# Kernel optimization log

Hardware: AMD Instinct MI355X
Metric: run time of the kernel (lower is better)

The kernel has to match this reference:

```python
import jax, jax.numpy as jnp
import numpy as np

N, F, E, LIN, C, B = 16384, 500, 128, 128, 10, 4096
P_EDGE = 0.002  # ~32 avg degree


def _l2norm(x):
    # F.normalize(dim=1), eps=1e-12
    n = jnp.linalg.norm(x, axis=1, keepdims=True)
    return x / jnp.maximum(n, 1e-12)


def setup_inputs() -> dict:
    key = jax.random.key(0)
    ks = jax.random.split(key, 10)
    adj = (jax.random.uniform(ks[0], (N, N)) < P_EDGE).astype(jnp.float32)
    idx = jnp.arange(N)
    adj = adj.at[idx, idx].set(1.0)  # self-loops guarantee degree >= 1
    data = jax.random.normal(ks[1], (N, F), dtype=jnp.float32)
    nodes = jax.random.randint(ks[2], (B,), 0, N)
    # Encoder 1: Linear(2F -> E); Encoder 2: Linear(2E -> E); classifier heads
    W1 = jax.random.normal(ks[3], (E, 2 * F), dtype=jnp.float32) * 0.03
    b1 = jnp.zeros((E,), jnp.float32)
    W2 = jax.random.normal(ks[4], (E, 2 * E), dtype=jnp.float32) * 0.06
    b2 = jnp.zeros((E,), jnp.float32)
    Wl1 = jax.random.normal(ks[5], (LIN, E), dtype=jnp.float32) * 0.08
    bl1 = jnp.zeros((LIN,), jnp.float32)
    Wl2 = jax.random.normal(ks[6], (C, LIN), dtype=jnp.float32) * 0.12
    bl2 = jnp.zeros((C,), jnp.float32)
    return {"nodes": nodes, "adj": adj, "data": data,
            "W1": W1, "b1": b1, "W2": W2, "b2": b2,
            "Wl1": Wl1, "bl1": bl1, "Wl2": Wl2, "bl2": bl2}


def reference(nodes, adj, data, W1, b1, W2, b2, Wl1, bl1, Wl2, bl2):
    deg = jnp.sum(adj, axis=1, keepdims=True)  # [N,1]
    # Layer 1 (mean aggregator over full neighbor set): computed for all nodes
    neigh1 = (adj @ data) / deg                               # [N,F]
    h1 = jnp.concatenate([data, neigh1], axis=1)              # [N,2F] (self, neigh)
    H1 = _l2norm(jax.nn.relu(h1 @ W1.T + b1))                 # [N,E]
    # Layer 2: only for the queried node batch
    neigh2 = (adj[nodes] @ H1) / deg[nodes]                   # [B,E]
    h2 = jnp.concatenate([H1[nodes], neigh2], axis=1)         # [B,2E]
    H2 = _l2norm(jax.nn.relu(h2 @ W2.T + b2))                 # [B,E]
    x = H2 @ Wl1.T + bl1                                      # [B,LIN]
    x = x @ Wl2.T + bl2                                       # [B,C]
    return jax.nn.softmax(x, axis=1)
```

## Files before the change

kernel.cpp:

```cpp
#include <hip/hip_runtime.h>
#include <math.h>
#include <stddef.h>

#define N_NODES 16384
#define F_DIM   500
#define KP1     512
#define E_DIM   128
#define C_DIM   10
#define B_DIM   4096
#define MAXDEG  128

typedef __attribute__((ext_vector_type(8))) short short8;
typedef __attribute__((ext_vector_type(4))) float f32x4;

__device__ inline unsigned short f2bf(float f) {
    union { float f; unsigned int u; } v; v.f = f;
    unsigned int u = v.u;
    u += 0x7FFFu + ((u >> 16) & 1u);
    return (unsigned short)(u >> 16);
}
__device__ inline float bf2f(unsigned short u) {
    union { unsigned int u; float f; } v; v.u = (unsigned int)u << 16;
    return v.f;
}

__global__ __launch_bounds__(256) void k_prep(const float* __restrict__ W1,
                                              const float* __restrict__ W2,
                                              const float* __restrict__ Wl1,
                                              unsigned short* __restrict__ Wt1,
                                              unsigned short* __restrict__ W2ab16,
                                              unsigned short* __restrict__ W2bb16,
                                              float* __restrict__ Wl1t) {
    const int bb = blockIdx.x;
    const int t = threadIdx.x;
    if (bb < 512) {
        int idx = bb * 256 + t;
        int n = idx >> 9, k = idx & 511;
        float v = (k < F_DIM) ? W1[(size_t)(n & 127) * 1000 + (n >> 7) * F_DIM + k] : 0.0f;
        Wt1[idx] = f2bf(v);
    } else if (bb < 576) {
        int idx = (bb - 512) * 256 + t;
        int n = idx >> 7, k = idx & 127;
        W2ab16[idx] = f2bf(W2[(size_t)n * 256 + k]);
    } else if (bb < 640) {
        int idx = (bb - 576) * 256 + t;
        int n = idx >> 7, k = idx & 127;
        W2bb16[idx] = f2bf(W2[(size_t)n * 256 + 128 + k]);
    } else {
        __shared__ float tile[32][33];
        int tb = bb - 640;
        int k0 = (tb & 3) * 32, e0 = (tb >> 2) * 32;
        int tx = t & 31, ty0 = t >> 5;
#pragma unroll
        for (int q = 0; q < 4; ++q) {
            int ty = ty0 + q * 8;
            tile[ty][tx] = Wl1[(size_t)(e0 + ty) * 128 + k0 + tx];
        }
        __syncthreads();
#pragma unroll
        for (int q = 0; q < 4; ++q) {
            int ty = ty0 + q * 8;
            Wl1t[(size_t)(k0 + ty) * 128 + e0 + tx] = tile[tx][ty];
        }
    }
}

__global__ __launch_bounds__(256) void k_mix(const float* __restrict__ data,
                                             const unsigned short* __restrict__ Wt1,
                                             unsigned short* __restrict__ Xb16,
                                             const float* __restrict__ adj,
                                             unsigned short* __restrict__ nbr,
                                             int* __restrict__ deg) {
    __shared__ alignas(16) unsigned char s_raw[(32 * 40 + 256 * 40) * 2];
    const int bb = blockIdx.x;
    const int tid = threadIdx.x;

    if (bb < 512) {
        unsigned short* sA = (unsigned short*)s_raw;
        unsigned short* sB = sA + 32 * 40;
        const int w    = tid >> 6;
        const int lane = tid & 63;
        const int l16  = lane & 15;
        const int quad = lane >> 4;
        const int blockM = bb * 32;
        f32x4 acc[2][4] = {};
#pragma unroll 1
        for (int c = 0; c < (KP1 >> 5); ++c) {
            const int k0 = c << 5;
            if (tid < 128) {
                int row = tid >> 2, cc = tid & 3;
                int kbase = k0 + cc * 8;
                const float* Arow = data + (size_t)(blockM + row) * F_DIM;
                float4 f0 = (kbase + 4 <= F_DIM) ? *(const float4*)(Arow + kbase)
                                                 : make_float4(0.f, 0.f, 0.f, 0.f);
                float4 f1 = (kbase + 8 <= F_DIM) ? *(const float4*)(Arow + kbase + 4)
                                                 : make_float4(0.f, 0.f, 0.f, 0.f);
                short8 v;
                v[0] = (short)f2bf(f0.x); v[1] = (short)f2bf(f0.y);
                v[2] = (short)f2bf(f0.z); v[3] = (short)f2bf(f0.w);
                v[4] = (short)f2bf(f1.x); v[5] = (short)f2bf(f1.y);
                v[6] = (short)f2bf(f1.z); v[7] = (short)f2bf(f1.w);
                *(short8*)(sA + row * 40 + cc * 8) = v;
            }
#pragma unroll
            for (int q = 0; q < 4; ++q) {
                int idx = tid + 256 * q;
                int row = idx >> 2, cc = idx & 3;
                short8 v = *(const short8*)(Wt1 + (size_t)row * KP1 + k0 + cc * 8);
                *(short8*)(sB + row * 40 + cc * 8) = v;
            }
            __syncthreads();
            short8 af[2], bf[4];
#pragma unroll
            for (int mt = 0; mt < 2; ++mt)
                af[mt] = *(const short8*)(sA + (mt * 16 + l16) * 40 + quad * 8);
#pragma unroll
            for (int nt = 0; nt < 4; ++nt)
                bf[nt] = *(const short8*)(sB + (w * 64 + nt * 16 + l16) * 40 + quad * 8);
#pragma unroll
            for (int mt = 0; mt < 2; ++mt)
#pragma unroll
                for (int nt = 0; nt < 4; ++nt)
                    acc[mt][nt] = __builtin_amdgcn_mfma_f32_16x16x32_bf16(af[mt], bf[nt], acc[mt][nt], 0, 0, 0);
            __syncthreads();
        }
#pragma unroll
        for (int mt = 0; mt < 2; ++mt)
#pragma unroll
            for (int nt = 0; nt < 4; ++nt) {
                int col = w * 64 + nt * 16 + l16;
#pragma unroll
                for (int r = 0; r < 4; ++r) {
                    int row = blockM + mt * 16 + quad * 4 + r;
                    Xb16[(size_t)row * 256 + col] = f2bf(acc[mt][nt][r]);
                }
            }
    } else {
        const int i = bb - 512;
        int* s_cnt = (int*)s_raw;
        int* s_idx = ((int*)s_raw) + 4;
        const float4* row4 = (const float4*)(adj + (size_t)i * N_NODES);
        if (tid == 0) *s_cnt = 0;
        __syncthreads();
        float4 v[16];
#pragma unroll
        for (int p = 0; p < 16; ++p) v[p] = row4[p * 256 + tid];
#pragma unroll
        for (int p = 0; p < 16; ++p) {
            int col = p * 1024 + tid * 4;
            if (v[p].x != 0.f) { int q = atomicAdd(s_cnt, 1); if (q < MAXDEG) s_idx[q] = col;     }
            if (v[p].y != 0.f) { int q = atomicAdd(s_cnt, 1); if (q < MAXDEG) s_idx[q] = col + 1; }
            if (v[p].z != 0.f) { int q = atomicAdd(s_cnt, 1); if (q < MAXDEG) s_idx[q] = col + 2; }
            if (v[p].w != 0.f) { int q = atomicAdd(s_cnt, 1); if (q < MAXDEG) s_idx[q] = col + 3; }
        }
        __syncthreads();
        int cnt = *s_cnt; if (cnt > MAXDEG) cnt = MAXDEG;
        if (tid < cnt) nbr[(size_t)i * MAXDEG + tid] = (unsigned short)s_idx[tid];
        if (tid == 0) deg[i] = cnt;
    }
}

__global__ __launch_bounds__(256) void k_gather(const unsigned short* __restrict__ nbr,
                                                const int* __restrict__ deg,
                                                const unsigned short* __restrict__ Xb16,
                                                const float* __restrict__ b1,
                                                unsigned short* __restrict__ H1b) {
    const int i = blockIdx.x;
    const int t = threadIdx.x;
    const int cnt = deg[i];
    __shared__ int s_idx[MAXDEG];
    __shared__ float s_part[8][128];
    __shared__ float s_w[2];
    if (t < cnt) s_idx[t] = nbr[(size_t)i * MAXDEG + t];
    __syncthreads();
    const int g = t >> 5, l = t & 31;
    float4 a4 = make_float4(0.f, 0.f, 0.f, 0.f);
    for (int k = g; k < cnt; k += 8) {
        ushort4 x4 = ((const ushort4*)(Xb16 + (size_t)s_idx[k] * 256 + 128))[l];
        a4.x += bf2f(x4.x); a4.y += bf2f(x4.y); a4.z += bf2f(x4.z); a4.w += bf2f(x4.w);
    }
    *(float4*)&s_part[g][l * 4] = a4;
    __syncthreads();
    float vv = 0.f;
    if (t < 128) {
        float tot = 0.f;
#pragma unroll
        for (int g2 = 0; g2 < 8; ++g2) tot += s_part[g2][t];
        vv = bf2f(Xb16[(size_t)i * 256 + t]) + tot / (float)cnt + b1[t];
        vv = fmaxf(vv, 0.f);
        float s = vv * vv;
#pragma unroll
        for (int off = 32; off > 0; off >>= 1) s += __shfl_down(s, off, 64);
        if ((t & 63) == 0) s_w[t >> 6] = s;
    }
    __syncthreads();
    if (t < 128) {
        float denom = fmaxf(sqrtf(s_w[0] + s_w[1]), 1e-12f);
        H1b[(size_t)i * 128 + t] = f2bf(vv / denom);
    }
}

__global__ __launch_bounds__(256) void k_gemm2(const unsigned short* __restrict__ H1b,
                                               const unsigned short* __restrict__ W2bb16,
                                               const unsigned short* __restrict__ W2ab16,
                                               const int* __restrict__ nodes,
                                               unsigned short* __restrict__ Yb16,
                                               float* __restrict__ Ya) {
    __shared__ unsigned short sA[32 * 40];
    __shared__ unsigned short sB[128 * 40];
    const int bb = blockIdx.x;
    const bool selfp = (bb >= 512);
    const unsigned short* B = selfp ? W2ab16 : W2bb16;
    const int blockM = (selfp ? (bb - 512) : bb) * 32;
    const int tid  = threadIdx.x;
    const int w    = tid >> 6;
    const int lane = tid & 63;
    const int l16  = lane & 15;
    const int quad = lane >> 4;
    f32x4 acc[2][2] = {};
#pragma unroll
    for (int c = 0; c < 4; ++c) {
        const int k0 = c << 5;
        if (tid < 128) {
            int row = tid >> 2, cc = tid & 3;
            int m = blockM + row;
            int src = selfp ? nodes[m] : m;
            short8 v = *(const short8*)(H1b + (size_t)src * 128 + k0 + cc * 8);
            *(short8*)(sA + row * 40 + cc * 8) = v;
        }
#pragma unroll
        for (int q = 0; q < 2; ++q) {
            int idx = tid + 256 * q;
            int row = idx >> 2, cc = idx & 3;
            short8 v = *(const short8*)(B + (size_t)row * 128 + k0 + cc * 8);
            *(short8*)(sB + row * 40 + cc * 8) = v;
        }
        __syncthreads();
        short8 af[2], bf[2];
#pragma unroll
        for (int mt = 0; mt < 2; ++mt)
            af[mt] = *(const short8*)(sA + (mt * 16 + l16) * 40 + quad * 8);
#pragma unroll
        for (int nt = 0; nt < 2; ++nt)
            bf[nt] = *(const short8*)(sB + (w * 32 + nt * 16 + l16) * 40 + quad * 8);
#pragma unroll
        for (int mt = 0; mt < 2; ++mt)
#pragma unroll
            for (int nt = 0; nt < 2; ++nt)
                acc[mt][nt] = __builtin_amdgcn_mfma_f32_16x16x32_bf16(af[mt], bf[nt], acc[mt][nt], 0, 0, 0);
        __syncthreads();
    }
#pragma unroll
    for (int mt = 0; mt < 2; ++mt)
#pragma unroll
        for (int nt = 0; nt < 2; ++nt) {
            int col = w * 32 + nt * 16 + l16;
#pragma unroll
            for (int r = 0; r < 4; ++r) {
                int row = blockM + mt * 16 + quad * 4 + r;
                if (selfp) Ya[(size_t)row * 128 + col] = acc[mt][nt][r];
                else       Yb16[(size_t)row * 128 + col] = f2bf(acc[mt][nt][r]);
            }
        }
}

__global__ __launch_bounds__(256) void k_l2head(const int* __restrict__ nodes,
                                                const unsigned short* __restrict__ nbr,
                                                const int* __restrict__ deg,
                                                const unsigned short* __restrict__ Yb16,
                                                const float* __restrict__ Ya,
                                                const float* __restrict__ b2,
                                                const float* __restrict__ Wl1t,
                                                const float* __restrict__ bl1,
                                                const float* __restrict__ Wl2,
                                                const float* __restrict__ bl2,
                                                float* __restrict__ out) {
    const int b = blockIdx.x;
    const int t = threadIdx.x;
    const int n = nodes[b];
    const int cnt = deg[n];
    __shared__ int s_idx[MAXDEG];
    __shared__ float s_part[8][128];
    __shared__ float s_h[128];
    __shared__ float s_x[128];
    __shared__ float s_c[C_DIM];
    __shared__ float s_w[2];
    if (t < cnt) s_idx[t] = nbr[(size_t)n * MAXDEG + t];
    __syncthreads();
    const int g = t >> 5, l = t & 31;
    float4 a4 = make_float4(0.f, 0.f, 0.f, 0.f);
    for (int k = g; k < cnt; k += 8) {
        ushort4 y4 = ((const ushort4*)(Yb16 + (size_t)s_idx[k] * 128))[l];
        a4.x += bf2f(y4.x); a4.y += bf2f(y4.y); a4.z += bf2f(y4.z); a4.w += bf2f(y4.w);
    }
    *(float4*)&s_part[g][l * 4] = a4;
    __syncthreads();
    float vv = 0.f;
    if (t < 128) {
        float tot = 0.f;
#pragma unroll
        for (int g2 = 0; g2 < 8; ++g2) tot += s_part[g2][t];
        vv = Ya[(size_t)b * 128 + t] + tot / (float)cnt + b2[t];
        vv = fmaxf(vv, 0.f);
        float s = vv * vv;
#pragma unroll
        for (int off = 32; off > 0; off >>= 1) s += __shfl_down(s, off, 64);
        if ((t & 63) == 0) s_w[t >> 6] = s;
    }
    __syncthreads();
    if (t < 128) {
        float denom = fmaxf(sqrtf(s_w[0] + s_w[1]), 1e-12f);
        s_h[t] = vv / denom;
    }
    __syncthreads();
    if (t < 128) {
        float x1 = bl1[t];
#pragma unroll 8
        for (int kk = 0; kk < 128; ++kk)
            x1 += Wl1t[kk * 128 + t] * s_h[kk];
        s_x[t] = x1;
    }
    __syncthreads();
    if (t < C_DIM) {
        float l2 = bl2[t];
        const float* wr = Wl2 + (size_t)t * 128;
        for (int kk = 0; kk < 128; ++kk) l2 += wr[kk] * s_x[kk];
        s_c[t] = l2;
    }
    __syncthreads();
    if (t < C_DIM) {
        float mx = -1e30f;
        for (int c = 0; c < C_DIM; ++c) mx = fmaxf(mx, s_c[c]);
        float se = 0.f;
        for (int c = 0; c < C_DIM; ++c) se += expf(s_c[c] - mx);
        out[(size_t)b * C_DIM + t] = expf(s_c[t] - mx) / se;
    }
}

extern "C" void kernel_launch(void* const* d_in, const int* in_sizes, int n_in,
                              void* d_out, int out_size, void* d_ws, size_t ws_size,
                              hipStream_t stream) {
    const int*   nodes = (const int*)  d_in[0];
    const float* adj   = (const float*)d_in[1];
    const float* data  = (const float*)d_in[2];
    const float* W1    = (const float*)d_in[3];
    const float* b1    = (const float*)d_in[4];
    const float* W2    = (const float*)d_in[5];
    const float* b2    = (const float*)d_in[6];
    const float* Wl1   = (const float*)d_in[7];
    const float* bl1   = (const float*)d_in[8];
    const float* Wl2   = (const float*)d_in[9];
    const float* bl2   = (const float*)d_in[10];
    float* out = (float*)d_out;

    float* Wl1t = (float*)d_ws;
    float* Ya   = Wl1t + 16384;
    unsigned short* Wt1    = (unsigned short*)(Ya + (size_t)B_DIM * 128);
    unsigned short* W2ab16 = Wt1 + 256 * KP1;
    unsigned short* W2bb16 = W2ab16 + 16384;
    unsigned short* Xb16   = W2bb16 + 16384;
    unsigned short* H1b    = Xb16 + (size_t)N_NODES * 256;
    unsigned short* Yb16   = H1b + (size_t)N_NODES * 128;
    unsigned short* nbr    = Yb16 + (size_t)N_NODES * 128;
    int* deg = (int*)(nbr + (size_t)N_NODES * MAXDEG);

    k_prep<<<656, 256, 0, stream>>>(W1, W2, Wl1, Wt1, W2ab16, W2bb16, Wl1t);

    k_mix   <<<512 + N_NODES, 256, 0, stream>>>(data, Wt1, Xb16, adj, nbr, deg);
    k_gather<<<N_NODES, 256, 0, stream>>>(nbr, deg, Xb16, b1, H1b);

    k_gemm2 <<<512 + 128, 256, 0, stream>>>(H1b, W2bb16, W2ab16, nodes, Yb16, Ya);

    k_l2head<<<B_DIM, 256, 0, stream>>>(nodes, nbr, deg, Yb16, Ya, b2,
                                        Wl1t, bl1, Wl2, bl2, out);
}
```

Before: 1.419 ms.

## Fuse weight prep into first GEMM and use wave-per-node gather and head

Merges the weight-prep kernel into the first GEMM/adjacency-scan kernel. The GEMM now reads fp32 data and W1 straight from global memory into registers and converts to bf16 there, with no LDS staging or barriers. The neighbor gather and classifier head kernels switch from one 256-thread block per node to one wavefront per node, using shuffles in place of shared-memory reductions. The second GEMM likewise loads its operands directly into registers without LDS. This removes a launch, the Wt1 buffer and many syncthreads, at the cost of redundant global loads and bf16 conversions of W1 in every GEMM block.

```diff
diff --git a/kernel.cpp b/kernel.cpp
--- a/kernel.cpp
+++ b/kernel.cpp
@@ -4,7 +4,6 @@
 
 #define N_NODES 16384
 #define F_DIM   500
-#define KP1     512
 #define E_DIM   128
 #define C_DIM   10
 #define B_DIM   4096
@@ -23,34 +22,45 @@
     union { unsigned int u; float f; } v; v.u = (unsigned int)u << 16;
     return v.f;
 }
-
-__global__ __launch_bounds__(256) void k_prep(const float* __restrict__ W1,
-                                              const float* __restrict__ W2,
-                                              const float* __restrict__ Wl1,
-                                              unsigned short* __restrict__ Wt1,
-                                              unsigned short* __restrict__ W2ab16,
-                                              unsigned short* __restrict__ W2bb16,
-                                              float* __restrict__ Wl1t) {
+__device__ inline short8 cvt8(float4 a, float4 b) {
+    short8 v;
+    v[0] = (short)f2bf(a.x); v[1] = (short)f2bf(a.y);
+    v[2] = (short)f2bf(a.z); v[3] = (short)f2bf(a.w);
+    v[4] = (short)f2bf(b.x); v[5] = (short)f2bf(b.y);
+    v[6] = (short)f2bf(b.z); v[7] = (short)f2bf(b.w);
+    return v;
+}
+
+__global__ __launch_bounds__(256) void k_fuse1(const float* __restrict__ data,
+                                               const float* __restrict__ W1,
+                                               const float* __restrict__ W2,
+                                               const float* __restrict__ Wl1,
+                                               const float* __restrict__ adj,
+                                               unsigned short* __restrict__ Xb16,
+                                               unsigned short* __restrict__ nbr,
+                                               int* __restrict__ deg,
+                                               unsigned short* __restrict__ W2ab16,
+                                               unsigned short* __restrict__ W2bb16,
+                                               float* __restrict__ Wl1t) {
+    __shared__ alignas(16) unsigned char smem[4352];
     const int bb = blockIdx.x;
-    const int t = threadIdx.x;
-    if (bb < 512) {
-        int idx = bb * 256 + t;
-        int n = idx >> 9, k = idx & 511;
-        float v = (k < F_DIM) ? W1[(size_t)(n & 127) * 1000 + (n >> 7) * F_DIM + k] : 0.0f;
-        Wt1[idx] = f2bf(v);
-    } else if (bb < 576) {
-        int idx = (bb - 512) * 256 + t;
+    const int tid = threadIdx.x;
+
+    if (bb < 64) {
+        int idx = bb * 256 + tid;
         int n = idx >> 7, k = idx & 127;
         W2ab16[idx] = f2bf(W2[(size_t)n * 256 + k]);
-    } else if (bb < 640) {
-        int idx = (bb - 576) * 256 + t;
+        return;
+    } else if (bb < 128) {
+        int idx = (bb - 64) * 256 + tid;
         int n = idx >> 7, k = idx & 127;
         W2bb16[idx] = f2bf(W2[(size_t)n * 256 + 128 + k]);
-    } else {
-        __shared__ float tile[32][33];
-        int tb = bb - 640;
+        return;
+    } else if (bb < 144) {
+        float (*tile)[33] = (float (*)[33])smem;
+        int tb = bb - 128;
         int k0 = (tb & 3) * 32, e0 = (tb >> 2) * 32;
-        int tx = t & 31, ty0 = t >> 5;
+        int tx = tid & 31, ty0 = tid >> 5;
 #pragma unroll
         for (int q = 0; q < 4; ++q) {
             int ty = ty0 + q * 8;
@@ -62,67 +72,41 @@
             int ty = ty0 + q * 8;
             Wl1t[(size_t)(k0 + ty) * 128 + e0 + tx] = tile[tx][ty];
         }
-    }
-}
-
-__global__ __launch_bounds__(256) void k_mix(const float* __restrict__ data,
-                                             const unsigned short* __restrict__ Wt1,
-                                             unsigned short* __restrict__ Xb16,
-                                             const float* __restrict__ adj,
-                                             unsigned short* __restrict__ nbr,
-                                             int* __restrict__ deg) {
-    __shared__ alignas(16) unsigned char s_raw[(32 * 40 + 256 * 40) * 2];
-    const int bb = blockIdx.x;
-    const int tid = threadIdx.x;
-
-    if (bb < 512) {
-        unsigned short* sA = (unsigned short*)s_raw;
-        unsigned short* sB = sA + 32 * 40;
+        return;
+    } else if (bb < 656) {
+        const int g = bb - 144;
+        const int blockM = g * 32;
         const int w    = tid >> 6;
         const int lane = tid & 63;
         const int l16  = lane & 15;
         const int quad = lane >> 4;
-        const int blockM = bb * 32;
         f32x4 acc[2][4] = {};
-#pragma unroll 1
-        for (int c = 0; c < (KP1 >> 5); ++c) {
-            const int k0 = c << 5;
-            if (tid < 128) {
-                int row = tid >> 2, cc = tid & 3;
-                int kbase = k0 + cc * 8;
-                const float* Arow = data + (size_t)(blockM + row) * F_DIM;
-                float4 f0 = (kbase + 4 <= F_DIM) ? *(const float4*)(Arow + kbase)
-                                                 : make_float4(0.f, 0.f, 0.f, 0.f);
-                float4 f1 = (kbase + 8 <= F_DIM) ? *(const float4*)(Arow + kbase + 4)
-                                                 : make_float4(0.f, 0.f, 0.f, 0.f);
-                short8 v;
-                v[0] = (short)f2bf(f0.x); v[1] = (short)f2bf(f0.y);
-                v[2] = (short)f2bf(f0.z); v[3] = (short)f2bf(f0.w);
-                v[4] = (short)f2bf(f1.x); v[5] = (short)f2bf(f1.y);
-                v[6] = (short)f2bf(f1.z); v[7] = (short)f2bf(f1.w);
-                *(short8*)(sA + row * 40 + cc * 8) = v;
+#pragma unroll 2
+        for (int c = 0; c < 16; ++c) {
+            const int kq = (c << 5) + quad * 8;
+            const bool ok0 = (kq + 4 <= F_DIM);
+            const bool ok1 = (kq + 8 <= F_DIM);
+            short8 af[2], bfr[4];
+#pragma unroll
+            for (int mt = 0; mt < 2; ++mt) {
+                const float* ap = data + (size_t)(blockM + mt * 16 + l16) * F_DIM + kq;
+                float4 f0 = ok0 ? *(const float4*)ap       : make_float4(0.f, 0.f, 0.f, 0.f);
+                float4 f1 = ok1 ? *(const float4*)(ap + 4) : make_float4(0.f, 0.f, 0.f, 0.f);
+                af[mt] = cvt8(f0, f1);
             }
 #pragma unroll
-            for (int q = 0; q < 4; ++q) {
-                int idx = tid + 256 * q;
-                int row = idx >> 2, cc = idx & 3;
-                short8 v = *(const short8*)(Wt1 + (size_t)row * KP1 + k0 + cc * 8);
-                *(short8*)(sB + row * 40 + cc * 8) = v;
+            for (int nt = 0; nt < 4; ++nt) {
+                int n = w * 64 + nt * 16 + l16;
+                const float* bp = W1 + (size_t)(n & 127) * 1000 + (n >> 7) * F_DIM + kq;
+                float4 g0 = ok0 ? *(const float4*)bp       : make_float4(0.f, 0.f, 0.f, 0.f);
+                float4 g1 = ok1 ? *(const float4*)(bp + 4) : make_float4(0.f, 0.f, 0.f, 0.f);
+                bfr[nt] = cvt8(g0, g1);
             }
-            __syncthreads();
-            short8 af[2], bf[4];
 #pragma unroll
             for (int mt = 0; mt < 2; ++mt)
-                af[mt] = *(const short8*)(sA + (mt * 16 + l16) * 40 + quad * 8);
-#pragma unroll
-            for (int nt = 0; nt < 4; ++nt)
-                bf[nt] = *(const short8*)(sB + (w * 64 + nt * 16 + l16) * 40 + quad * 8);
-#pragma unroll
-            for (int mt = 0; mt < 2; ++mt)
 #pragma unroll
                 for (int nt = 0; nt < 4; ++nt)
-                    acc[mt][nt] = __builtin_amdgcn_mfma_f32_16x16x32_bf16(af[mt], bf[nt], acc[mt][nt], 0, 0, 0);
-            __syncthreads();
+                    acc[mt][nt] = __builtin_amdgcn_mfma_f32_16x16x32_bf16(af[mt], bfr[nt], acc[mt][nt], 0, 0, 0);
         }
 #pragma unroll
         for (int mt = 0; mt < 2; ++mt)
@@ -136,9 +120,9 @@
                 }
             }
     } else {
-        const int i = bb - 512;
-        int* s_cnt = (int*)s_raw;
-        int* s_idx = ((int*)s_raw) + 4;
+        const int i = bb - 656;
+        int* s_cnt = (int*)smem;
+        int* s_idx = ((int*)smem) + 4;
         const float4* row4 = (const float4*)(adj + (size_t)i * N_NODES);
         if (tid == 0) *s_cnt = 0;
         __syncthreads();
@@ -165,38 +149,39 @@
                                                 const unsigned short* __restrict__ Xb16,
                                                 const float* __restrict__ b1,
                                                 unsigned short* __restrict__ H1b) {
-    const int i = blockIdx.x;
-    const int t = threadIdx.x;
+    const int lane = threadIdx.x & 63;
+    const int i = blockIdx.x * 4 + (threadIdx.x >> 6);
     const int cnt = deg[i];
-    __shared__ int s_idx[MAXDEG];
-    __shared__ float s_part[8][128];
-    __shared__ float s_w[2];
-    if (t < cnt) s_idx[t] = nbr[(size_t)i * MAXDEG + t];
-    __syncthreads();
-    const int g = t >> 5, l = t & 31;
-    float4 a4 = make_float4(0.f, 0.f, 0.f, 0.f);
-    for (int k = g; k < cnt; k += 8) {
-        ushort4 x4 = ((const ushort4*)(Xb16 + (size_t)s_idx[k] * 256 + 128))[l];
-        a4.x += bf2f(x4.x); a4.y += bf2f(x4.y); a4.z += bf2f(x4.z); a4.w += bf2f(x4.w);
-    }
-    *(float4*)&s_part[g][l * 4] = a4;
-    __syncthreads();
-    float vv = 0.f;
-    if (t < 128) {
-        float tot = 0.f;
-#pragma unroll
-        for (int g2 = 0; g2 < 8; ++g2) tot += s_part[g2][t];
-        vv = bf2f(Xb16[(size_t)i * 256 + t]) + tot / (float)cnt + b1[t];
-        vv = fmaxf(vv, 0.f);
-        float s = vv * vv;
-#pragma unroll
-        for (int off = 32; off > 0; off >>= 1) s += __shfl_down(s, off, 64);
-        if ((t & 63) == 0) s_w[t >> 6] = s;
-    }
-    __syncthreads();
-    if (t < 128) {
-        float denom = fmaxf(sqrtf(s_w[0] + s_w[1]), 1e-12f);
-        H1b[(size_t)i * 128 + t] = f2bf(vv / denom);
+    const int myn  = (lane < cnt)      ? (int)nbr[(size_t)i * MAXDEG + lane]      : 0;
+    const int myn2 = (lane + 64 < cnt) ? (int)nbr[(size_t)i * MAXDEG + lane + 64] : 0;
+    const int half = lane >> 5, l32 = lane & 31;
+    float ax = 0.f, ay = 0.f, az = 0.f, aw = 0.f;
+    for (int k = half; k < cnt; k += 2) {
+        int kk = k & 63;
+        int j1 = __shfl(myn, kk);
+        int j2 = __shfl(myn2, kk);
+        int j = (k < 64) ? j1 : j2;
+        ushort4 x4 = *(const ushort4*)(Xb16 + (size_t)j * 256 + 128 + l32 * 4);
+        ax += bf2f(x4.x); ay += bf2f(x4.y); az += bf2f(x4.z); aw += bf2f(x4.w);
+    }
+    ax += __shfl_xor(ax, 32); ay += __shfl_xor(ay, 32);
+    az += __shfl_xor(az, 32); aw += __shfl_xor(aw, 32);
+    ushort4 sx = *(const ushort4*)(Xb16 + (size_t)i * 256 + l32 * 4);
+    float4 bb = *(const float4*)(b1 + l32 * 4);
+    float fc = (float)cnt;
+    float v0 = fmaxf(bf2f(sx.x) + ax / fc + bb.x, 0.f);
+    float v1 = fmaxf(bf2f(sx.y) + ay / fc + bb.y, 0.f);
+    float v2 = fmaxf(bf2f(sx.z) + az / fc + bb.z, 0.f);
+    float v3 = fmaxf(bf2f(sx.w) + aw / fc + bb.w, 0.f);
+    float s = v0 * v0 + v1 * v1 + v2 * v2 + v3 * v3;
+#pragma unroll
+    for (int off = 16; off > 0; off >>= 1) s += __shfl_xor(s, off);
+    float rden = 1.0f / fmaxf(sqrtf(s), 1e-12f);
+    if (half == 0) {
+        ushort4 o;
+        o.x = f2bf(v0 * rden); o.y = f2bf(v1 * rden);
+        o.z = f2bf(v2 * rden); o.w = f2bf(v3 * rden);
+        *(ushort4*)(H1b + (size_t)i * 128 + l32 * 4) = o;
     }
 }
 
@@ -206,8 +191,6 @@
                                                const int* __restrict__ nodes,
                                                unsigned short* __restrict__ Yb16,
                                                float* __restrict__ Ya) {
-    __shared__ unsigned short sA[32 * 40];
-    __shared__ unsigned short sB[128 * 40];
     const int bb = blockIdx.x;
     const bool selfp = (bb >= 512);
     const unsigned short* B = selfp ? W2ab16 : W2bb16;
@@ -217,39 +200,29 @@
     const int lane = tid & 63;
     const int l16  = lane & 15;
     const int quad = lane >> 4;
+    int rsrc0 = blockM + l16,      rsrc1 = blockM + 16 + l16;
+    if (selfp) { rsrc0 = nodes[rsrc0]; rsrc1 = nodes[rsrc1]; }
+    short8 af[2][4], bfr[2][4];
+#pragma unroll
+    for (int c = 0; c < 4; ++c) {
+        af[0][c] = *(const short8*)(H1b + (size_t)rsrc0 * 128 + c * 32 + quad * 8);
+        af[1][c] = *(const short8*)(H1b + (size_t)rsrc1 * 128 + c * 32 + quad * 8);
+    }
+#pragma unroll
+    for (int nt = 0; nt < 2; ++nt) {
+        int n = w * 32 + nt * 16 + l16;
+#pragma unroll
+        for (int c = 0; c < 4; ++c)
+            bfr[nt][c] = *(const short8*)(B + (size_t)n * 128 + c * 32 + quad * 8);
+    }
     f32x4 acc[2][2] = {};
 #pragma unroll
-    for (int c = 0; c < 4; ++c) {
-        const int k0 = c << 5;
-        if (tid < 128) {
-            int row = tid >> 2, cc = tid & 3;
-            int m = blockM + row;
-            int src = selfp ? nodes[m] : m;
-            short8 v = *(const short8*)(H1b + (size_t)src * 128 + k0 + cc * 8);
-            *(short8*)(sA + row * 40 + cc * 8) = v;
-        }
-#pragma unroll
-        for (int q = 0; q < 2; ++q) {
-            int idx = tid + 256 * q;
-            int row = idx >> 2, cc = idx & 3;
-            short8 v = *(const short8*)(B + (size_t)row * 128 + k0 + cc * 8);
-            *(short8*)(sB + row * 40 + cc * 8) = v;
-        }
-        __syncthreads();
-        short8 af[2], bf[2];
+    for (int c = 0; c < 4; ++c)
 #pragma unroll
         for (int mt = 0; mt < 2; ++mt)
-            af[mt] = *(const short8*)(sA + (mt * 16 + l16) * 40 + quad * 8);
-#pragma unroll
-        for (int nt = 0; nt < 2; ++nt)
-            bf[nt] = *(const short8*)(sB + (w * 32 + nt * 16 + l16) * 40 + quad * 8);
-#pragma unroll
-        for (int mt = 0; mt < 2; ++mt)
 #pragma unroll
             for (int nt = 0; nt < 2; ++nt)
-                acc[mt][nt] = __builtin_amdgcn_mfma_f32_16x16x32_bf16(af[mt], bf[nt], acc[mt][nt], 0, 0, 0);
-        __syncthreads();
-    }
+                acc[mt][nt] = __builtin_amdgcn_mfma_f32_16x16x32_bf16(af[mt][c], bfr[nt][c], acc[mt][nt], 0, 0, 0);
 #pragma unroll
     for (int mt = 0; mt < 2; ++mt)
 #pragma unroll
@@ -275,66 +248,68 @@
                                                 const float* __restrict__ Wl2,
                                                 const float* __restrict__ bl2,
                                                 float* __restrict__ out) {
-    const int b = blockIdx.x;
-    const int t = threadIdx.x;
+    const int lane = threadIdx.x & 63;
+    const int b = blockIdx.x * 4 + (threadIdx.x >> 6);
     const int n = nodes[b];
     const int cnt = deg[n];
-    __shared__ int s_idx[MAXDEG];
-    __shared__ float s_part[8][128];
-    __shared__ float s_h[128];
-    __shared__ float s_x[128];
-    __shared__ float s_c[C_DIM];
-    __shared__ float s_w[2];
-    if (t < cnt) s_idx[t] = nbr[(size_t)n * MAXDEG + t];
-    __syncthreads();
-    const int g = t >> 5, l = t & 31;
-    float4 a4 = make_float4(0.f, 0.f, 0.f, 0.f);
-    for (int k = g; k < cnt; k += 8) {
-        ushort4 y4 = ((const ushort4*)(Yb16 + (size_t)s_idx[k] * 128))[l];
-        a4.x += bf2f(y4.x); a4.y += bf2f(y4.y); a4.z += bf2f(y4.z); a4.w += bf2f(y4.w);
-    }
-    *(float4*)&s_part[g][l * 4] = a4;
-    __syncthreads();
-    float vv = 0.f;
-    if (t < 128) {
-        float tot = 0.f;
-#pragma unroll
-        for (int g2 = 0; g2 < 8; ++g2) tot += s_part[g2][t];
-        vv = Ya[(size_t)b * 128 + t] + tot / (float)cnt + b2[t];
-        vv = fmaxf(vv, 0.f);
-        float s = vv * vv;
-#pragma unroll
-        for (int off = 32; off > 0; off >>= 1) s += __shfl_down(s, off, 64);
-        if ((t & 63) == 0) s_w[t >> 6] = s;
-    }
-    __syncthreads();
-    if (t < 128) {
-        float denom = fmaxf(sqrtf(s_w[0] + s_w[1]), 1e-12f);
-        s_h[t] = vv / denom;
-    }
-    __syncthreads();
-    if (t < 128) {
-        float x1 = bl1[t];
-#pragma unroll 8
-        for (int kk = 0; kk < 128; ++kk)
-            x1 += Wl1t[kk * 128 + t] * s_h[kk];
-        s_x[t] = x1;
-    }
-    __syncthreads();
-    if (t < C_DIM) {
-        float l2 = bl2[t];
-        const float* wr = Wl2 + (size_t)t * 128;
-        for (int kk = 0; kk < 128; ++kk) l2 += wr[kk] * s_x[kk];
-        s_c[t] = l2;
-    }
-    __syncthreads();
-    if (t < C_DIM) {
-        float mx = -1e30f;
-        for (int c = 0; c < C_DIM; ++c) mx = fmaxf(mx, s_c[c]);
-        float se = 0.f;
-        for (int c = 0; c < C_DIM; ++c) se += expf(s_c[c] - mx);
-        out[(size_t)b * C_DIM + t] = expf(s_c[t] - mx) / se;
-    }
+    const int myn  = (lane < cnt)      ? (int)nbr[(size_t)n * MAXDEG + lane]      : 0;
+    const int myn2 = (lane + 64 < cnt) ? (int)nbr[(size_t)n * MAXDEG + lane + 64] : 0;
+    const int half = lane >> 5, l32 = lane & 31;
+    float ax = 0.f, ay = 0.f, az = 0.f, aw = 0.f;
+    for (int k = half; k < cnt; k += 2) {
+        int kk = k & 63;
+        int j1 = __shfl(myn, kk);
+        int j2 = __shfl(myn2, kk);
+        int j = (k < 64) ? j1 : j2;
+        ushort4 y4 = *(const ushort4*)(Yb16 + (size_t)j * 128 + l32 * 4);
+        ax += bf2f(y4.x); ay += bf2f(y4.y); az += bf2f(y4.z); aw += bf2f(y4.w);
+    }
+    ax += __shfl_xor(ax, 32); ay += __shfl_xor(ay, 32);
+    az += __shfl_xor(az, 32); aw += __shfl_xor(aw, 32);
+    float4 ya = *(const float4*)(Ya + (size_t)b * 128 + l32 * 4);
+    float4 bb = *(const float4*)(b2 + l32 * 4);
+    float fc = (float)cnt;
+    float h0 = fmaxf(ya.x + ax / fc + bb.x, 0.f);
+    float h1 = fmaxf(ya.y + ay / fc + bb.y, 0.f);
+    float h2 = fmaxf(ya.z + az / fc + bb.z, 0.f);
+    float h3 = fmaxf(ya.w + aw / fc + bb.w, 0.f);
+    float s = h0 * h0 + h1 * h1 + h2 * h2 + h3 * h3;
+#pragma unroll
+    for (int off = 16; off > 0; off >>= 1) s += __shfl_xor(s, off);
+    float rden = 1.0f / fmaxf(sqrtf(s), 1e-12f);
+    h0 *= rden; h1 *= rden; h2 *= rden; h3 *= rden;
+    float2 bl = *(const float2*)(bl1 + 2 * lane);
+    float x0 = bl.x, x1 = bl.y;
+    const float* wl = Wl1t + 2 * lane;
+    for (int m = 0; m < 32; ++m) {
+        float k0 = __shfl(h0, m), k1 = __shfl(h1, m), k2 = __shfl(h2, m), k3 = __shfl(h3, m);
+        float2 w0 = *(const float2*)(wl + (size_t)(m * 4 + 0) * 128);
+        float2 w1 = *(const float2*)(wl + (size_t)(m * 4 + 1) * 128);
+        float2 w2 = *(const float2*)(wl + (size_t)(m * 4 + 2) * 128);
+        float2 w3 = *(const float2*)(wl + (size_t)(m * 4 + 3) * 128);
+        x0 += k0 * w0.x + k1 * w1.x + k2 * w2.x + k3 * w3.x;
+        x1 += k0 * w0.y + k1 * w1.y + k2 * w2.y + k3 * w3.y;
+    }
+    float cv[C_DIM];
+#pragma unroll
+    for (int cc = 0; cc < C_DIM; ++cc) {
+        float2 w = *(const float2*)(Wl2 + (size_t)cc * 128 + 2 * lane);
+        float p = x0 * w.x + x1 * w.y;
+#pragma unroll
+        for (int off = 32; off > 0; off >>= 1) p += __shfl_xor(p, off);
+        cv[cc] = p + bl2[cc];
+    }
+    float mx = cv[0];
+#pragma unroll
+    for (int cc = 1; cc < C_DIM; ++cc) mx = fmaxf(mx, cv[cc]);
+    float se = 0.f;
+#pragma unroll
+    for (int cc = 0; cc < C_DIM; ++cc) { cv[cc] = expf(cv[cc] - mx); se += cv[cc]; }
+    float rse = 1.0f / se;
+    float o = cv[0];
+#pragma unroll
+    for (int cc = 1; cc < C_DIM; ++cc) o = (lane == cc) ? cv[cc] : o;
+    if (lane < C_DIM) out[(size_t)b * C_DIM + lane] = o * rse;
 }
 
 extern "C" void kernel_launch(void* const* d_in, const int* in_sizes, int n_in,
@@ -355,8 +330,7 @@
 
     float* Wl1t = (float*)d_ws;
     float* Ya   = Wl1t + 16384;
-    unsigned short* Wt1    = (unsigned short*)(Ya + (size_t)B_DIM * 128);
-    unsigned short* W2ab16 = Wt1 + 256 * KP1;
+    unsigned short* W2ab16 = (unsigned short*)(Ya + (size_t)B_DIM * 128);
     unsigned short* W2bb16 = W2ab16 + 16384;
     unsigned short* Xb16   = W2bb16 + 16384;
     unsigned short* H1b    = Xb16 + (size_t)N_NODES * 256;
@@ -364,13 +338,11 @@
     unsigned short* nbr    = Yb16 + (size_t)N_NODES * 128;
     int* deg = (int*)(nbr + (size_t)N_NODES * MAXDEG);
 
-    k_prep<<<656, 256, 0, stream>>>(W1, W2, Wl1, Wt1, W2ab16, W2bb16, Wl1t);
-
-    k_mix   <<<512 + N_NODES, 256, 0, stream>>>(data, Wt1, Xb16, adj, nbr, deg);
-    k_gather<<<N_NODES, 256, 0, stream>>>(nbr, deg, Xb16, b1, H1b);
-
-    k_gemm2 <<<512 + 128, 256, 0, stream>>>(H1b, W2bb16, W2ab16, nodes, Yb16, Ya);
-
-    k_l2head<<<B_DIM, 256, 0, stream>>>(nodes, nbr, deg, Yb16, Ya, b2,
-                                        Wl1t, bl1, Wl2, bl2, out);
-}
+    k_fuse1<<<144 + 512 + N_NODES, 256, 0, stream>>>(data, W1, W2, Wl1, adj,
+                                                     Xb16, nbr, deg,
+                                                     W2ab16, W2bb16, Wl1t);
+    k_gather<<<N_NODES / 4, 256, 0, stream>>>(nbr, deg, Xb16, b1, H1b);
+    k_gemm2<<<512 + 128, 256, 0, stream>>>(H1b, W2bb16, W2ab16, nodes, Yb16, Ya);
+    k_l2head<<<B_DIM / 4, 256, 0, stream>>>(nodes, nbr, deg, Yb16, Ya, b2,
+                                            Wl1t, bl1, Wl2, bl2, out);
+}
```

Result: no change. 1.443 ms (+1.7%).
